# Optimization experiments

Measured on AMD Instinct MI355X. Metric: run time of the kernel, lower is better.

## Reference

```python
import jax, jax.numpy as jnp
import numpy as np

B, C, T, K, DIL = 8, 1024, 8192, 4, 1
PAD = (K - 1) * DIL

def setup_inputs() -> dict:
    key = jax.random.key(0)
    k1, k2, k3 = jax.random.split(key, 3)
    x = jax.random.normal(k1, (B, C, T), dtype=jnp.float32)
    # torch Conv1d depthwise weight: (C, 1, K), bias: (C,)
    fan_in = K  # in_channels/groups * K = 1 * K
    bound = 1.0 / np.sqrt(fan_in)
    w = jax.random.uniform(k2, (C, 1, K), dtype=jnp.float32, minval=-bound, maxval=bound)
    b = jax.random.uniform(k3, (C,), dtype=jnp.float32, minval=-bound, maxval=bound)
    return {"x": x, "w": w, "b": b}

def reference(x, w, b):
    # Causal depthwise conv1d: left-pad by (K-1)*dilation, groups=C.
    y = jax.lax.conv_general_dilated(
        x, w,
        window_strides=(1,),
        padding=[(PAD, 0)],
        rhs_dilation=(DIL,),
        dimension_numbers=("NCH", "OIH", "NCH"),
        feature_group_count=C,
    )
    return y + b[None, :, None]
```

## Files before the change

### kernel.cpp

```cpp
#include <hip/hip_runtime.h>


constexpr int Bc = 8;
constexpr int Cc = 1024;
constexpr int Tc = 8192;

__global__ __launch_bounds__(256) void dwconv1d_kernel(
    const float* __restrict__ x,
    const float* __restrict__ w,
    const float* __restrict__ bias,
    float* __restrict__ y,
    int n4)
{
    const float4* __restrict__ x4 = reinterpret_cast<const float4*>(x);
    const float4* __restrict__ w4 = reinterpret_cast<const float4*>(w);
    float4* __restrict__ y4 = reinterpret_cast<float4*>(y);

    const int stride = gridDim.x * blockDim.x;
    for (int idx = blockIdx.x * blockDim.x + threadIdx.x; idx < n4; idx += stride) {
        const int p   = idx << 2;
        const int row = p >> 13;
        const int t0  = p & (Tc - 1);
        const int c   = row & (Cc - 1);

        float4 cur = x4[idx];
        float4 prev = make_float4(0.f, 0.f, 0.f, 0.f);
        if (t0 != 0) prev = x4[idx - 1];

        const float4 wc = w4[c];
        const float bc  = bias[c];

        float4 out;
        out.x = fmaf(wc.x, prev.y, fmaf(wc.y, prev.z, fmaf(wc.z, prev.w, fmaf(wc.w, cur.x, bc))));
        out.y = fmaf(wc.x, prev.z, fmaf(wc.y, prev.w, fmaf(wc.z, cur.x,  fmaf(wc.w, cur.y, bc))));
        out.z = fmaf(wc.x, prev.w, fmaf(wc.y, cur.x,  fmaf(wc.z, cur.y,  fmaf(wc.w, cur.z, bc))));
        out.w = fmaf(wc.x, cur.x,  fmaf(wc.y, cur.y,  fmaf(wc.z, cur.z,  fmaf(wc.w, cur.w, bc))));

        y4[idx] = out;
    }
}

extern "C" void kernel_launch(void* const* d_in, const int* in_sizes, int n_in,
                              void* d_out, int out_size, void* d_ws, size_t ws_size,
                              hipStream_t stream) {
    const float* x    = (const float*)d_in[0];
    const float* w    = (const float*)d_in[1];
    const float* bias = (const float*)d_in[2];
    float* y = (float*)d_out;

    const int n4 = (Bc * Cc * Tc) / 4;
    const int block = 256;
    const int grid = 2048;
    dwconv1d_kernel<<<grid, block, 0, stream>>>(x, w, bias, y, n4);
}
```

Measured before the change: 106.8 us.

## Map one block per row and share neighbor values via wave shuffles

Each block now handles one (batch,channel) row, loading eight float4 values per thread up front. Each lane takes the previous-element data from the neighbouring lane with shuffles rather than issuing a second global load, and only lane 0 of each wave loads the boundary float4. This cuts redundant load traffic and raises loads in flight per thread, at the cost of more registers and shuffle instructions.

```diff
diff --git a/kernel.cpp b/kernel.cpp
--- a/kernel.cpp
+++ b/kernel.cpp
@@ -1,42 +1,54 @@
 #include <hip/hip_runtime.h>
 
 
-constexpr int Bc = 8;
 constexpr int Cc = 1024;
-constexpr int Tc = 8192;
+constexpr int T4 = 2048;
 
 __global__ __launch_bounds__(256) void dwconv1d_kernel(
     const float* __restrict__ x,
     const float* __restrict__ w,
     const float* __restrict__ bias,
-    float* __restrict__ y,
-    int n4)
+    float* __restrict__ y)
 {
-    const float4* __restrict__ x4 = reinterpret_cast<const float4*>(x);
-    const float4* __restrict__ w4 = reinterpret_cast<const float4*>(w);
-    float4* __restrict__ y4 = reinterpret_cast<float4*>(y);
+    const int row = blockIdx.x;
+    const int c   = row & (Cc - 1);
 
-    const int stride = gridDim.x * blockDim.x;
-    for (int idx = blockIdx.x * blockDim.x + threadIdx.x; idx < n4; idx += stride) {
-        const int p   = idx << 2;
-        const int row = p >> 13;
-        const int t0  = p & (Tc - 1);
-        const int c   = row & (Cc - 1);
+    const float4* __restrict__ xr = reinterpret_cast<const float4*>(x) + (size_t)row * T4;
+    float4* __restrict__ yr       = reinterpret_cast<float4*>(y) + (size_t)row * T4;
 
-        float4 cur = x4[idx];
-        float4 prev = make_float4(0.f, 0.f, 0.f, 0.f);
-        if (t0 != 0) prev = x4[idx - 1];
+    const float4 wc = reinterpret_cast<const float4*>(w)[c];
+    const float  bc = bias[c];
 
-        const float4 wc = w4[c];
-        const float bc  = bias[c];
+    const int tid  = threadIdx.x;
+    const int lane = tid & 63;
+
+    float4 cur[8];
+#pragma unroll
+    for (int j = 0; j < 8; ++j)
+        cur[j] = xr[tid + j * 256];
+
+#pragma unroll
+    for (int j = 0; j < 8; ++j) {
+        const int idx = tid + j * 256;
+
+        const int wave_base = (tid & ~63) + j * 256;
+        float4 bp = make_float4(0.f, 0.f, 0.f, 0.f);
+        if (wave_base != 0) bp = xr[wave_base - 1];
+
+        float py = __shfl_up(cur[j].y, 1);
+        float pz = __shfl_up(cur[j].z, 1);
+        float pw = __shfl_up(cur[j].w, 1);
+        py = (lane == 0) ? bp.y : py;
+        pz = (lane == 0) ? bp.z : pz;
+        pw = (lane == 0) ? bp.w : pw;
 
         float4 out;
-        out.x = fmaf(wc.x, prev.y, fmaf(wc.y, prev.z, fmaf(wc.z, prev.w, fmaf(wc.w, cur.x, bc))));
-        out.y = fmaf(wc.x, prev.z, fmaf(wc.y, prev.w, fmaf(wc.z, cur.x,  fmaf(wc.w, cur.y, bc))));
-        out.z = fmaf(wc.x, prev.w, fmaf(wc.y, cur.x,  fmaf(wc.z, cur.y,  fmaf(wc.w, cur.z, bc))));
-        out.w = fmaf(wc.x, cur.x,  fmaf(wc.y, cur.y,  fmaf(wc.z, cur.z,  fmaf(wc.w, cur.w, bc))));
+        out.x = fmaf(wc.x, py,       fmaf(wc.y, pz,       fmaf(wc.z, pw,       fmaf(wc.w, cur[j].x, bc))));
+        out.y = fmaf(wc.x, pz,       fmaf(wc.y, pw,       fmaf(wc.z, cur[j].x, fmaf(wc.w, cur[j].y, bc))));
+        out.z = fmaf(wc.x, pw,       fmaf(wc.y, cur[j].x, fmaf(wc.z, cur[j].y, fmaf(wc.w, cur[j].z, bc))));
+        out.w = fmaf(wc.x, cur[j].x, fmaf(wc.y, cur[j].y,  fmaf(wc.z, cur[j].z, fmaf(wc.w, cur[j].w, bc))));
 
-        y4[idx] = out;
+        yr[idx] = out;
     }
 }
 
@@ -48,8 +60,6 @@
     const float* bias = (const float*)d_in[2];
     float* y = (float*)d_out;
 
-    const int n4 = (Bc * Cc * Tc) / 4;
-    const int block = 256;
-    const int grid = 2048;
-    dwconv1d_kernel<<<grid, block, 0, stream>>>(x, w, bias, y, n4);
+    const int rows = 8 * Cc;
+    dwconv1d_kernel<<<rows, 256, 0, stream>>>(x, w, bias, y);
 }
```

After: 100.4 us. 6.0% less time.
